# Optimization experiments

Measured on AMD Instinct MI355X. Metric: run time of the kernel, lower is better.

## Reference

```python
import jax, jax.numpy as jnp
import numpy as np

MAX_COC = 50.0
NUM_PLANES = 32
KERNEL_CAP = 31
B, C, H, W = 4, 3, 512, 512


def _plane_kernels():
    """Static per-plane Gaussian kernels, mirroring the torch loop exactly."""
    planes = np.linspace(0.0, MAX_COC, NUM_PLANES)
    kernels = []
    for coc in planes:
        if coc < 0.5:
            kernels.append(None)  # identity (no blur)
            continue
        sigma = coc / 2.355
        k = int(2 * coc + 1)
        if k % 2 == 0:
            k += 1
        k = min(k, KERNEL_CAP)
        coords = np.arange(k, dtype=np.float32) - k // 2
        g = np.exp(-coords ** 2 / (2.0 * sigma ** 2)).astype(np.float32)
        g = g / g.sum()
        kernels.append(np.outer(g, g).astype(np.float32))
    return planes, kernels


def _depthwise_blur(x, kern2d):
    # x: [B,C,H,W]; kern2d: [k,k] shared across channels (grouped conv, groups=C)
    c = x.shape[1]
    k = kern2d.shape[0]
    w = jnp.broadcast_to(jnp.asarray(kern2d, dtype=x.dtype)[None, None], (c, 1, k, k))
    return jax.lax.conv_general_dilated(
        x, w, window_strides=(1, 1), padding=[(k // 2, k // 2)] * 2,
        dimension_numbers=('NCHW', 'OIHW', 'NCHW'), feature_group_count=c)


def setup_inputs() -> dict:
    key = jax.random.key(0)
    k1, k2 = jax.random.split(key)
    sharp_image = jax.random.uniform(k1, (B, C, H, W), dtype=jnp.float32)
    # CoC in pixels, spanning the full [0, MAX_COC) range so all 32 bins fire
    coc_map = jax.random.uniform(k2, (B, 1, H, W), dtype=jnp.float32) * MAX_COC
    return {"sharp_image": sharp_image, "coc_map": coc_map}


def reference(sharp_image, coc_map):
    """Spatially-varying defocus blur: per-plane Gaussian blur + hard-binned blend."""
    planes, kernels = _plane_kernels()
    result = jnp.zeros_like(sharp_image)
    for i in range(NUM_PLANES):
        blurred = sharp_image if kernels[i] is None else _depthwise_blur(sharp_image, kernels[i])
        if i == 0:
            w = coc_map <= (planes[0] + planes[1]) / 2
        elif i == NUM_PLANES - 1:
            w = coc_map > (planes[-2] + planes[-1]) / 2
        else:
            lower = (planes[i - 1] + planes[i]) / 2
            upper = (planes[i] + planes[i + 1]) / 2
            w = (coc_map > lower) & (coc_map <= upper)
        # incremental masked blend (same math as stack-then-sum, less memory)
        result = result + blurred * w.astype(sharp_image.dtype)
    return result
```

## Files before the change

### kernel.cpp

```cpp
#include <hip/hip_runtime.h>
#include <math.h>

typedef _Float16 h2_t __attribute__((ext_vector_type(2)));
typedef _Float16 h4_t __attribute__((ext_vector_type(4)));
typedef _Float16 h8_t __attribute__((ext_vector_type(8)));

#define NP 32
#define KC 31
#define HH 512
#define WW 512
#define BB 4
#define CC 3

#define TXO 64
#define TYO 32
#define NT 512
#define TROWS 62
#define TWORDS 48
#define WSTR 36

__device__ h2_t g_wtabh[NP * WSTR];

__global__ void init_wtab_kernel() {
    const int tid = threadIdx.x;
    const int p = tid >> 5;
    const int t = tid & 31;
    const double stepd = 50.0 / 31.0;
    double coc = (p < 31) ? (double)p * stepd : 50.0;
    float gt;
    if (coc < 0.5) {
        gt = (t == 15) ? 1.f : 0.f;
    } else {
        double sigma = coc / 2.355;
        int k = (int)(2.0 * coc + 1.0);
        if ((k & 1) == 0) k += 1;
        if (k > KC) k = KC;
        int h = k / 2;
        int d = t - 15;
        float denom = (float)(2.0 * sigma * sigma);
        float v = (d >= -h && d <= h && t < KC) ? expf(-(float)(d * d) / denom) : 0.f;
        float s = v;
        #pragma unroll
        for (int off = 1; off < 32; off <<= 1) s += __shfl_xor(s, off, 32);
        gt = v / s;
    }
    const int m = t & 15;
    const int s0 = (t < 16) ? (2 * m) : ((2 * m - 1 < 0) ? 0 : 2 * m - 1);
    const int s1 = (t < 16) ? (2 * m + 1) : (2 * m);
    float w0 = __shfl(gt, s0, 32);
    float w1 = __shfl(gt, s1, 32);
    if (t >= 16 && (2 * m - 1) < 0) w0 = 0.f;
    h2_t w; w.x = (_Float16)w0; w.y = (_Float16)w1;
    g_wtabh[p * WSTR + t] = w;
    if (t < WSTR - 32) {
        h2_t z; z.x = (_Float16)0.f; z.y = (_Float16)0.f;
        g_wtabh[p * WSTR + 32 + t] = z;
    }
}

__device__ __forceinline__ double plane_of(int i) {
    const double stepd = 50.0 / 31.0;
    return (i < 31) ? (double)i * stepd : 50.0;
}

__launch_bounds__(512, 2)
__global__ void defocus_kernel(const float* __restrict__ img,
                               const float* __restrict__ coc,
                               float* __restrict__ out) {
    const int tx = threadIdx.x;
    const int ty = threadIdx.y;
    const int tid = ty * 16 + tx;
    const int tilex = blockIdx.x * TXO;
    const int tiley = blockIdx.y * TYO;
    const int b = blockIdx.z;

    __shared__ __align__(16) h2_t wtab[NP * WSTR];
    __shared__ __align__(16) h2_t tile[TROWS * TWORDS];

    for (int f = tid; f < NP * WSTR; f += NT) wtab[f] = g_wtabh[f];

    const int yo = tiley + ty;
    const int xo = tilex + tx * 4;

    const float4 cv = *(const float4*)&coc[((size_t)b * HH + yo) * WW + xo];
    const float cocf[4] = {cv.x, cv.y, cv.z, cv.w};
    int idx[4];
    #pragma unroll
    for (int j = 0; j < 4; ++j) {
        const double stepd = 50.0 / 31.0;
        double cd = (double)cocf[j];
        int i0 = (int)floor(cd / stepd + 0.5);
        i0 = min(max(i0, 0), 31);
        if (i0 > 0 && cd <= 0.5 * (plane_of(i0 - 1) + plane_of(i0))) {
            i0 -= 1;
        } else if (i0 < 31 && cd > 0.5 * (plane_of(i0) + plane_of(i0 + 1))) {
            i0 += 1;
        }
        idx[j] = i0;
    }

    __syncthreads();

    h2_t wj[4][16];
    #pragma unroll
    for (int j = 0; j < 4; ++j) {
        const h2_t* wp = &wtab[idx[j] * WSTR + (j & 1) * 16];
        #pragma unroll
        for (int m = 0; m < 4; ++m) {
            h8_t v = *(const h8_t*)(wp + 4 * m);
            #pragma unroll
            for (int q = 0; q < 4; ++q) {
                h2_t t; t.x = v[2 * q]; t.y = v[2 * q + 1];
                wj[j][4 * m + q] = t;
            }
        }
    }

    for (int c = 0; c < CC; ++c) {
        __syncthreads();
        const float* src = img + (size_t)(b * CC + c) * HH * WW;
        for (int f = tid; f < TROWS * TWORDS; f += NT) {
            int r = f / TWORDS;
            int w = f - r * TWORDS;
            int gy = tiley - 15 + r;
            int gx = tilex - 15 + 2 * w;
            float v0 = 0.f, v1 = 0.f;
            if ((unsigned)gy < (unsigned)HH) {
                if ((unsigned)gx < (unsigned)WW) v0 = src[gy * WW + gx];
                if ((unsigned)(gx + 1) < (unsigned)WW) v1 = src[gy * WW + gx + 1];
            }
            h2_t pv; pv.x = (_Float16)v0; pv.y = (_Float16)v1;
            tile[f] = pv;
        }
        __syncthreads();

        float acc0 = 0.f, acc1 = 0.f, acc2 = 0.f, acc3 = 0.f;
        const h2_t* rowbase = &tile[ty * TWORDS + 2 * tx];
        #pragma unroll
        for (int dy = 0; dy < KC; ++dy) {
            const h2_t* rp = rowbase + dy * TWORDS;
            h2_t rw[18];
            #pragma unroll
            for (int m = 0; m < 9; ++m) {
                h4_t q = *(const h4_t*)(rp + 2 * m);
                h2_t lo; lo.x = q[0]; lo.y = q[1];
                h2_t hi; hi.x = q[2]; hi.y = q[3];
                rw[2 * m]     = lo;
                rw[2 * m + 1] = hi;
            }
            float rs0 = 0.f, rs1 = 0.f, rs2 = 0.f, rs3 = 0.f;
            #pragma unroll
            for (int m = 0; m < 16; ++m) {
                rs0 = __builtin_amdgcn_fdot2(wj[0][m], rw[m],     rs0, false);
                rs1 = __builtin_amdgcn_fdot2(wj[1][m], rw[m],     rs1, false);
                rs2 = __builtin_amdgcn_fdot2(wj[2][m], rw[m + 1], rs2, false);
                rs3 = __builtin_amdgcn_fdot2(wj[3][m], rw[m + 1], rs3, false);
            }
            float cw0, cw1, cw2, cw3;
            if ((dy & 1) == 0) {
                cw0 = (float)wj[0][dy >> 1].x;
                cw2 = (float)wj[2][dy >> 1].x;
                cw1 = (float)wj[1][dy >> 1].y;
                cw3 = (float)wj[3][dy >> 1].y;
            } else {
                cw0 = (float)wj[0][dy >> 1].y;
                cw2 = (float)wj[2][dy >> 1].y;
                cw1 = (float)wj[1][(dy + 1) >> 1].x;
                cw3 = (float)wj[3][(dy + 1) >> 1].x;
            }
            acc0 += cw0 * rs0;
            acc1 += cw1 * rs1;
            acc2 += cw2 * rs2;
            acc3 += cw3 * rs3;
        }

        *(float4*)&out[((size_t)(b * CC + c) * HH + yo) * WW + xo] =
            make_float4(acc0, acc1, acc2, acc3);
    }
}

extern "C" void kernel_launch(void* const* d_in, const int* in_sizes, int n_in,
                              void* d_out, int out_size, void* d_ws, size_t ws_size,
                              hipStream_t stream) {
    const float* sharp = (const float*)d_in[0];
    const float* cocm  = (const float*)d_in[1];
    float* out = (float*)d_out;

    init_wtab_kernel<<<1, 1024, 0, stream>>>();
    dim3 grid(WW / TXO, HH / TYO, BB);
    dim3 block(16, 32, 1);
    defocus_kernel<<<grid, block, 0, stream>>>(sharp, cocm, out);
}
```

Before: 136.8 us.

## Fuse weight-table init into main kernel and prefetch all channel tiles upfront

```diff
diff --git a/kernel.cpp b/kernel.cpp
--- a/kernel.cpp
+++ b/kernel.cpp
@@ -17,46 +17,9 @@
 #define NT 512
 #define TROWS 62
 #define TWORDS 48
+#define TILEW (TROWS * TWORDS)
 #define WSTR 36
 
-__device__ h2_t g_wtabh[NP * WSTR];
-
-__global__ void init_wtab_kernel() {
-    const int tid = threadIdx.x;
-    const int p = tid >> 5;
-    const int t = tid & 31;
-    const double stepd = 50.0 / 31.0;
-    double coc = (p < 31) ? (double)p * stepd : 50.0;
-    float gt;
-    if (coc < 0.5) {
-        gt = (t == 15) ? 1.f : 0.f;
-    } else {
-        double sigma = coc / 2.355;
-        int k = (int)(2.0 * coc + 1.0);
-        if ((k & 1) == 0) k += 1;
-        if (k > KC) k = KC;
-        int h = k / 2;
-        int d = t - 15;
-        float denom = (float)(2.0 * sigma * sigma);
-        float v = (d >= -h && d <= h && t < KC) ? expf(-(float)(d * d) / denom) : 0.f;
-        float s = v;
-        #pragma unroll
-        for (int off = 1; off < 32; off <<= 1) s += __shfl_xor(s, off, 32);
-        gt = v / s;
-    }
-    const int m = t & 15;
-    const int s0 = (t < 16) ? (2 * m) : ((2 * m - 1 < 0) ? 0 : 2 * m - 1);
-    const int s1 = (t < 16) ? (2 * m + 1) : (2 * m);
-    float w0 = __shfl(gt, s0, 32);
-    float w1 = __shfl(gt, s1, 32);
-    if (t >= 16 && (2 * m - 1) < 0) w0 = 0.f;
-    h2_t w; w.x = (_Float16)w0; w.y = (_Float16)w1;
-    g_wtabh[p * WSTR + t] = w;
-    if (t < WSTR - 32) {
-        h2_t z; z.x = (_Float16)0.f; z.y = (_Float16)0.f;
-        g_wtabh[p * WSTR + 32 + t] = z;
-    }
-}
 
 __device__ __forceinline__ double plane_of(int i) {
     const double stepd = 50.0 / 31.0;
@@ -75,14 +38,88 @@
     const int b = blockIdx.z;
 
     __shared__ __align__(16) h2_t wtab[NP * WSTR];
-    __shared__ __align__(16) h2_t tile[TROWS * TWORDS];
-
-    for (int f = tid; f < NP * WSTR; f += NT) wtab[f] = g_wtabh[f];
+    __shared__ __align__(16) h2_t tile[3 * TILEW];
 
     const int yo = tiley + ty;
     const int xo = tilex + tx * 4;
 
     const float4 cv = *(const float4*)&coc[((size_t)b * HH + yo) * WW + xo];
+
+    int foff[6]; int fr[6]; bool g0[6], g1[6];
+    #pragma unroll
+    for (int i = 0; i < 6; ++i) {
+        const int f = tid + i * NT;
+        const int r = f / TWORDS;
+        const int w = f - r * TWORDS;
+        const int gy = tiley - 15 + r;
+        const int gx = tilex - 15 + 2 * w;
+        const bool rowok = (f < TILEW) && ((unsigned)gy < (unsigned)HH);
+        g0[i] = rowok && ((unsigned)gx < (unsigned)WW);
+        g1[i] = rowok && ((unsigned)(gx + 1) < (unsigned)WW);
+        foff[i] = gy * WW + gx;
+        fr[i] = f;
+    }
+    float sv[3][6][2];
+    #pragma unroll
+    for (int c = 0; c < 3; ++c) {
+        const float* src = img + (size_t)(b * CC + c) * HH * WW;
+        #pragma unroll
+        for (int i = 0; i < 6; ++i) {
+            sv[c][i][0] = g0[i] ? src[foff[i]]     : 0.f;
+            sv[c][i][1] = g1[i] ? src[foff[i] + 1] : 0.f;
+        }
+    }
+
+    {
+        const int t = tid & 31;
+        #pragma unroll
+        for (int pass = 0; pass < 2; ++pass) {
+            const int p = (tid >> 5) + 16 * pass;
+            const double stepd = 50.0 / 31.0;
+            double cocp = (p < 31) ? (double)p * stepd : 50.0;
+            float gt;
+            if (cocp < 0.5) {
+                gt = (t == 15) ? 1.f : 0.f;
+            } else {
+                double sigma = cocp / 2.355;
+                int k = (int)(2.0 * cocp + 1.0);
+                if ((k & 1) == 0) k += 1;
+                if (k > KC) k = KC;
+                int h = k / 2;
+                int d = t - 15;
+                float denom = (float)(2.0 * sigma * sigma);
+                float v = (d >= -h && d <= h && t < KC) ? expf(-(float)(d * d) / denom) : 0.f;
+                float s = v;
+                #pragma unroll
+                for (int off = 1; off < 32; off <<= 1) s += __shfl_xor(s, off, 32);
+                gt = v / s;
+            }
+            const int m = t & 15;
+            const int s0 = (t < 16) ? (2 * m) : ((2 * m - 1 < 0) ? 0 : 2 * m - 1);
+            const int s1 = (t < 16) ? (2 * m + 1) : (2 * m);
+            float w0 = __shfl(gt, s0, 32);
+            float w1 = __shfl(gt, s1, 32);
+            if (t >= 16 && (2 * m - 1) < 0) w0 = 0.f;
+            h2_t w; w.x = (_Float16)w0; w.y = (_Float16)w1;
+            wtab[p * WSTR + t] = w;
+            if (t < WSTR - 32) {
+                h2_t z; z.x = (_Float16)0.f; z.y = (_Float16)0.f;
+                wtab[p * WSTR + 32 + t] = z;
+            }
+        }
+    }
+
+    #pragma unroll
+    for (int c = 0; c < 3; ++c) {
+        #pragma unroll
+        for (int i = 0; i < 6; ++i) {
+            if (fr[i] < TILEW) {
+                h2_t pv; pv.x = (_Float16)sv[c][i][0]; pv.y = (_Float16)sv[c][i][1];
+                tile[c * TILEW + fr[i]] = pv;
+            }
+        }
+    }
+
     const float cocf[4] = {cv.x, cv.y, cv.z, cv.w};
     int idx[4];
     #pragma unroll
@@ -110,32 +147,16 @@
             h8_t v = *(const h8_t*)(wp + 4 * m);
             #pragma unroll
             for (int q = 0; q < 4; ++q) {
-                h2_t t; t.x = v[2 * q]; t.y = v[2 * q + 1];
-                wj[j][4 * m + q] = t;
-            }
-        }
-    }
-
-    for (int c = 0; c < CC; ++c) {
-        __syncthreads();
-        const float* src = img + (size_t)(b * CC + c) * HH * WW;
-        for (int f = tid; f < TROWS * TWORDS; f += NT) {
-            int r = f / TWORDS;
-            int w = f - r * TWORDS;
-            int gy = tiley - 15 + r;
-            int gx = tilex - 15 + 2 * w;
-            float v0 = 0.f, v1 = 0.f;
-            if ((unsigned)gy < (unsigned)HH) {
-                if ((unsigned)gx < (unsigned)WW) v0 = src[gy * WW + gx];
-                if ((unsigned)(gx + 1) < (unsigned)WW) v1 = src[gy * WW + gx + 1];
-            }
-            h2_t pv; pv.x = (_Float16)v0; pv.y = (_Float16)v1;
-            tile[f] = pv;
-        }
-        __syncthreads();
-
+                h2_t t2; t2.x = v[2 * q]; t2.y = v[2 * q + 1];
+                wj[j][4 * m + q] = t2;
+            }
+        }
+    }
+
+    #pragma unroll 1
+    for (int c = 0; c < 3; ++c) {
         float acc0 = 0.f, acc1 = 0.f, acc2 = 0.f, acc3 = 0.f;
-        const h2_t* rowbase = &tile[ty * TWORDS + 2 * tx];
+        const h2_t* rowbase = &tile[c * TILEW + ty * TWORDS + 2 * tx];
         #pragma unroll
         for (int dy = 0; dy < KC; ++dy) {
             const h2_t* rp = rowbase + dy * TWORDS;
@@ -186,7 +207,6 @@
     const float* cocm  = (const float*)d_in[1];
     float* out = (float*)d_out;
 
-    init_wtab_kernel<<<1, 1024, 0, stream>>>();
     dim3 grid(WW / TXO, HH / TYO, BB);
     dim3 block(16, 32, 1);
     defocus_kernel<<<grid, block, 0, stream>>>(sharp, cocm, out);
```

Result: no change. 136.8 us (-0.0%).
